# Kernel tuning notes

Measured on AMD Instinct MI355X. Metric: run time of the kernel, lower is better.

## Reference

```python
import jax, jax.numpy as jnp
import numpy as np

NUM_NODES = 10000
WINDOW = 8
IN_C = 8
HID = 64
N_TOT = WINDOW * NUM_NODES
N_EDGES = 1280000
EPS = 1e-5


def setup_inputs() -> dict:
    key = jax.random.key(0)
    ks = jax.random.split(key, 12)
    s = 0.05
    X = jax.random.normal(ks[0], (N_TOT, IN_C), jnp.float32)
    edge_index = jax.random.randint(ks[1], (2, N_EDGES), 0, N_TOT, dtype=jnp.int32)
    edge_weight = jax.random.uniform(ks[2], (N_EDGES,), jnp.float32)
    return dict(
        X=X, edge_index=edge_index, edge_weight=edge_weight,
        w1=jax.random.normal(ks[3], (IN_C, HID), jnp.float32) * s, b1=jnp.zeros(HID, jnp.float32),
        w2=jax.random.normal(ks[4], (HID, HID), jnp.float32) * s, b2=jnp.zeros(HID, jnp.float32),
        g1=jnp.ones(HID, jnp.float32), be1=jnp.zeros(HID, jnp.float32),
        g2=jnp.ones(HID, jnp.float32), be2=jnp.zeros(HID, jnp.float32),
        wih1=jax.random.normal(ks[5], (4 * HID, 2 * HID), jnp.float32) * s,
        whh1=jax.random.normal(ks[6], (4 * HID, HID), jnp.float32) * s,
        bih1=jnp.zeros(4 * HID, jnp.float32), bhh1=jnp.zeros(4 * HID, jnp.float32),
        wih2=jax.random.normal(ks[7], (4 * HID, HID), jnp.float32) * s,
        whh2=jax.random.normal(ks[8], (4 * HID, HID), jnp.float32) * s,
        bih2=jnp.zeros(4 * HID, jnp.float32), bhh2=jnp.zeros(4 * HID, jnp.float32),
    )


def _gcn(x, src, dst, ew, w, b):
    h = x @ w
    deg = jax.ops.segment_sum(ew, dst, num_segments=N_TOT) + 1.0
    dinv = jax.lax.rsqrt(deg)
    norm = dinv[src] * ew * dinv[dst]                               # [E]
    agg = jax.ops.segment_sum(norm[:, None] * h[src], dst, num_segments=N_TOT)
    return agg + h * (dinv * dinv)[:, None] + b                      # self-loop term: h[i]/deg[i]


def _bn(x, g, b):
    # BatchNorm1d, training-mode batch statistics (biased variance)
    mu = x.mean(0)
    var = ((x - mu) ** 2).mean(0)
    return (x - mu) * jax.lax.rsqrt(var + EPS) * g + b


def _lstm(xs, wih, whh, bih, bhh):
    # xs: [T, B, F]; torch gate order i, f, g, o
    B = xs.shape[1]
    def step(carry, xt):
        h, c = carry
        z = xt @ wih.T + h @ whh.T + bih + bhh
        i, f, g, o = jnp.split(z, 4, axis=1)
        c = jax.nn.sigmoid(f) * c + jax.nn.sigmoid(i) * jnp.tanh(g)
        h = jax.nn.sigmoid(o) * jnp.tanh(c)
        return (h, c), h
    init = (jnp.zeros((B, HID), xs.dtype), jnp.zeros((B, HID), xs.dtype))
    (h, c), ys = jax.lax.scan(step, init, xs)
    return ys, h


def reference(X, edge_index, edge_weight, w1, b1, w2, b2, g1, be1, g2, be2,
              wih1, whh1, bih1, bhh1, wih2, whh2, bih2, bhh2):
    src, dst = edge_index[0], edge_index[1]
    # skip-feature S: [B*num_nodes, in_channels + window - 1]
    S = X.reshape(1, WINDOW, NUM_NODES, IN_C).transpose(0, 2, 1, 3).reshape(-1, WINDOW, IN_C)
    Sfeat = jnp.concatenate([S[:, 0, :], S[:, 1:, IN_C - 1]], axis=1)
    # two GCN layers (dropout omitted: deterministic baseline)
    x1 = _bn(jax.nn.relu(_gcn(X, src, dst, edge_weight, w1, b1)), g1, be1)
    x2 = _bn(jax.nn.relu(_gcn(x1, src, dst, edge_weight, w2, b2)), g2, be2)
    xc = jnp.concatenate([x1, x2], axis=1)                           # [N_TOT, 2H]
    xs = xc.reshape(1, WINDOW, NUM_NODES, 2 * HID).transpose(1, 0, 2, 3).reshape(WINDOW, -1, 2 * HID)
    ys, h1 = _lstm(xs, wih1, whh1, bih1, bhh1)
    ys2, h2 = _lstm(ys, wih2, whh2, bih2, bhh2)
    return jnp.concatenate([h1, h2, Sfeat], axis=1)                  # [num_nodes, 2H + IN_C + WINDOW - 1]
```

## Files before the change

kernel.cpp:

```cpp
#include <hip/hip_runtime.h>
#include <hip/hip_bf16.h>
#include <math.h>

#define NNODES 10000
#define NT     80000
#define NE     1280000
#define NBKT   625
#define CHUNK  5000
#define EPB    3072
#define BNEPS  1e-5f

typedef __bf16 bf16x8 __attribute__((ext_vector_type(8)));
typedef float  f32x4  __attribute__((ext_vector_type(4)));
typedef float  f32x2  __attribute__((ext_vector_type(2)));

__device__ __forceinline__ float frcp(float x){ return __builtin_amdgcn_rcpf(x); }
__device__ __forceinline__ float fsig(float x){ return frcp(1.0f + __expf(-x)); }
__device__ __forceinline__ float ftanh(float x){ return 1.0f - 2.0f*frcp(1.0f + __expf(2.0f*x)); }
__device__ __forceinline__ float u2f(unsigned int u){ union{unsigned int u; float f;} c; c.u=u; return c.f; }
__device__ __forceinline__ unsigned int f2u(float f){ union{float f; unsigned int u;} c; c.f=f; return c.u; }
__device__ __forceinline__ unsigned short f2bu(float v){ __hip_bfloat16 h = __float2bfloat16(v); return *(unsigned short*)&h; }
__device__ __forceinline__ unsigned int pk2(float a, float b){ return (unsigned int)f2bu(a) | ((unsigned int)f2bu(b) << 16); }
__device__ __forceinline__ float dec15(unsigned int p){ return u2f((p & 0x7fffu) << 17); }

__global__ __launch_bounds__(256) void prep_w_kernel(
    const float* __restrict__ wih1, const float* __restrict__ whh1,
    const float* __restrict__ bih1, const float* __restrict__ bhh1,
    const float* __restrict__ wih2, const float* __restrict__ whh2,
    const float* __restrict__ bih2, const float* __restrict__ bhh2,
    const float* __restrict__ w1g, const float* __restrict__ w2g,
    unsigned int* __restrict__ W1f, unsigned int* __restrict__ W2f,
    float* __restrict__ bs1, float* __restrict__ bs2,
    unsigned int* __restrict__ W2g, unsigned int* __restrict__ W1g)
{
    int gid = blockIdx.x*256 + threadIdx.x;
    if (gid < 24576) {
        int i = gid & 3, lane = (gid>>2)&63, rest = gid>>8;
        int ks = rest % 6; rest /= 6;
        int nt = rest & 3, w = rest >> 2;
        int gate = nt*64 + w*16 + (lane & 15);
        int k = ks*32 + ((lane>>4)&3)*8 + 2*i;
        float v0 = (k     < 128) ? wih1[gate*128 + k]       : whh1[gate*64 + (k-128)];
        float v1 = (k + 1 < 128) ? wih1[gate*128 + k + 1]   : whh1[gate*64 + (k+1-128)];
        W1f[gid] = pk2(v0, v1);
    } else if (gid < 40960) {
        int r = gid - 24576;
        int i = r & 3, lane = (r>>2)&63, rest = r>>8;
        int ks = rest & 3; rest >>= 2;
        int nt = rest & 3, w = rest >> 2;
        int gate = nt*64 + w*16 + (lane & 15);
        int k = ks*32 + ((lane>>4)&3)*8 + 2*i;
        float v0 = (k     < 64) ? wih2[gate*64 + k]     : whh2[gate*64 + (k-64)];
        float v1 = (k + 1 < 64) ? wih2[gate*64 + k + 1] : whh2[gate*64 + (k+1-64)];
        W2f[r] = pk2(v0, v1);
    } else if (gid < 41216) {
        int j = gid - 40960; bs1[j] = bih1[j] + bhh1[j];
    } else if (gid < 41472) {
        int j = gid - 41216; bs2[j] = bih2[j] + bhh2[j];
    } else if (gid < 43520) {
        int r = gid - 41472;
        int i = r & 3, lane = (r>>2)&63, rest = r>>8;
        int ks = rest & 1, w = rest >> 1;
        int col = w*16 + (lane & 15);
        int k = ks*32 + ((lane>>4)&3)*8 + 2*i;
        W2g[r] = pk2(w2g[k*64 + col], w2g[(k+1)*64 + col]);
    } else if (gid < 44544) {
        int r = gid - 43520;
        int i = r & 3, lane = (r>>2)&63, w = r>>8;
        int col = w*16 + (lane & 15);
        int k = ((lane>>4)&3)*8 + 2*i;
        float v0 = (k     < 8) ? w1g[k*64 + col]     : 0.f;
        float v1 = (k + 1 < 8) ? w1g[(k+1)*64 + col] : 0.f;
        W1g[r] = pk2(v0, v1);
    }
}

__global__ __launch_bounds__(256) void sortA1_kernel(const int* __restrict__ dst,
                                                     const float* __restrict__ X,
                                                     unsigned int* __restrict__ Xb,
                                                     int* __restrict__ histmat)
{
    __shared__ int h[NBKT];
    for (int i = threadIdx.x; i < NBKT; i += 256) h[i] = 0;
    __syncthreads();
    int base = blockIdx.x*CHUNK;
    for (int i = threadIdx.x; i < CHUNK; i += 256)
        atomicAdd(&h[dst[base + i] >> 7], 1);
    for (int i = threadIdx.x; i < 1250; i += 256) {
        int gid = blockIdx.x*1250 + i;
        float2 v = *(const float2*)&X[(size_t)gid*2];
        Xb[gid] = pk2(v.x, v.y);
    }
    __syncthreads();
    for (int i = threadIdx.x; i < NBKT; i += 256)
        histmat[blockIdx.x*640 + i] = h[i];
}

__global__ __launch_bounds__(256) void sortA2a_kernel(const int* __restrict__ histmat,
                                                      int* __restrict__ offmatT,
                                                      int* __restrict__ binTotal)
{
    __shared__ int v[256];
    int b = blockIdx.x, t = threadIdx.x;
    int x = histmat[t*640 + b];
    v[t] = x;
    __syncthreads();
    for (int off = 1; off < 256; off <<= 1) {
        int y = (t >= off) ? v[t-off] : 0;
        __syncthreads();
        v[t] += y;
        __syncthreads();
    }
    offmatT[b*256 + t] = v[t] - x;
    if (t == 255) binTotal[b] = v[255];
}

__global__ __launch_bounds__(1024) void sortA2b_kernel(const int* __restrict__ binTotal,
                                                       int* __restrict__ bucketbase,
                                                       int* __restrict__ rowptr)
{
    __shared__ int part[1024];
    int t = threadIdx.x;
    int v = (t < NBKT) ? binTotal[t] : 0;
    part[t] = v;
    __syncthreads();
    for (int off = 1; off < 1024; off <<= 1) {
        int y = (t >= off) ? part[t-off] : 0;
        __syncthreads();
        part[t] += y;
        __syncthreads();
    }
    if (t < NBKT) bucketbase[t] = part[t] - v;
    if (t == 0) { bucketbase[NBKT] = NE; rowptr[NT] = NE; }
}

__global__ __launch_bounds__(256) void sortA3_kernel(const int* __restrict__ src,
                                                     const int* __restrict__ dst,
                                                     const float* __restrict__ ew,
                                                     const int* __restrict__ offmatT,
                                                     const int* __restrict__ bucketbase,
                                                     uint2* __restrict__ esort)
{
    __shared__ int cur[NBKT];
    int blk = blockIdx.x;
    for (int i = threadIdx.x; i < NBKT; i += 256)
        cur[i] = bucketbase[i] + offmatT[i*256 + blk];
    __syncthreads();
    int base = blk*CHUNK;
    for (int i = threadIdx.x; i < CHUNK; i += 256) {
        int e = base + i;
        int d = dst[e];
        int pos = atomicAdd(&cur[d >> 7], 1);
        uint2 r;
        r.x = (unsigned int)src[e] | ((unsigned int)(d & 127) << 17);
        r.y = f2u(ew[e]);
        esort[pos] = r;
    }
}

__global__ __launch_bounds__(256) void sortB1_kernel(const int* __restrict__ bucketbase,
                                                     const uint2* __restrict__ esort,
                                                     unsigned char* __restrict__ urank,
                                                     int* __restrict__ rowptr,
                                                     float* __restrict__ dinv)
{
    __shared__ int cnt[128];
    __shared__ float dg[128];
    __shared__ int ptr[128];
    int bin = blockIdx.x, t = threadIdx.x;
    if (t < 128) { cnt[t] = 0; dg[t] = 0.f; }
    __syncthreads();
    int base = bucketbase[bin], end = bucketbase[bin+1];
    for (int i = base + t; i < end; i += 256) {
        uint2 r = esort[i];
        int dl = (r.x >> 17) & 127;
        int rk = atomicAdd(&cnt[dl], 1);
        atomicAdd(&dg[dl], u2f(r.y));
        urank[i] = (unsigned char)rk;
    }
    __syncthreads();
    if (t < 128) ptr[t] = cnt[t];
    __syncthreads();
    for (int off = 1; off < 128; off <<= 1) {
        int y = (t >= off && t < 128) ? ptr[t-off] : 0;
        __syncthreads();
        if (t < 128) ptr[t] += y;
        __syncthreads();
    }
    if (t < 128) {
        rowptr[bin*128 + t] = base + ptr[t] - cnt[t];
        dinv[bin*128 + t]   = rsqrtf(dg[t] + 1.0f);
    }
}

__global__ __launch_bounds__(256) void sortB2g8_kernel(const int* __restrict__ bucketbase,
                                                       const uint2* __restrict__ esort,
                                                       const unsigned char* __restrict__ urank,
                                                       const int* __restrict__ rowptr,
                                                       const float* __restrict__ dinv,
                                                       unsigned int* __restrict__ epack,
                                                       const uint4* __restrict__ Xb,
                                                       uint4* __restrict__ agg8b)
{
    __shared__ unsigned int eld[EPB];
    int bin = blockIdx.x;
    int base = bucketbase[bin], end = bucketbase[bin+1];
    int cnt = end - base;
    for (int i = threadIdx.x; i < cnt; i += 256) {
        uint2 r = esort[base + i];
        int s = r.x & 0x1FFFF;
        int d = bin*128 + ((r.x >> 17) & 127);
        float w = u2f(r.y) * dinv[s];
        unsigned int p15 = (f2u(w) + (1u << 16)) >> 17;
        unsigned int pv = ((unsigned int)s << 15) | p15;
        int pos = rowptr[d] + (int)urank[base + i];
        epack[pos] = pv;
        int lpos = pos - base;
        if (lpos < EPB) eld[lpos] = pv;
    }
    __syncthreads();
    int t = threadIdx.x;
    int dl = t >> 1, par = t & 1;
    int d = bin*128 + dl;
    int beg = rowptr[d], endd = rowptr[d+1];
    float acc[8];
    #pragma unroll
    for (int k = 0; k < 8; ++k) acc[k] = 0.f;
    for (int i = beg + par; i < endd; i += 2) {
        int lpos = i - base;
        unsigned int p = (lpos < EPB) ? eld[lpos] : epack[i];
        float nrm = dec15(p);
        uint4 xv = Xb[p >> 15];
        unsigned int um[4] = {xv.x, xv.y, xv.z, xv.w};
        #pragma unroll
        for (int m = 0; m < 4; ++m) {
            acc[2*m]   = fmaf(nrm, u2f(um[m] << 16),         acc[2*m]);
            acc[2*m+1] = fmaf(nrm, u2f(um[m] & 0xffff0000u), acc[2*m+1]);
        }
    }
    #pragma unroll
    for (int k = 0; k < 8; ++k) acc[k] += __shfl_xor(acc[k], 1);
    if (par == 0) {
        float dv = dinv[d];
        uint4 xd = Xb[d];
        unsigned int ud[4] = {xd.x, xd.y, xd.z, xd.w};
        #pragma unroll
        for (int m = 0; m < 4; ++m) {
            acc[2*m]   = dv * fmaf(dv, u2f(ud[m] << 16),         acc[2*m]);
            acc[2*m+1] = dv * fmaf(dv, u2f(ud[m] & 0xffff0000u), acc[2*m+1]);
        }
        agg8b[d] = make_uint4(pk2(acc[0],acc[1]), pk2(acc[2],acc[3]),
                              pk2(acc[4],acc[5]), pk2(acc[6],acc[7]));
    }
}

__global__ __launch_bounds__(256) void gemm8relu_kernel(const uint4* __restrict__ agg8b,
                                                        const unsigned int* __restrict__ W1g,
                                                        const float* __restrict__ b,
                                                        unsigned short* __restrict__ y,
                                                        float* __restrict__ sums)
{
    __shared__ __align__(16) unsigned short As[64][8];
    __shared__ float sm[256], sq[256];
    const int tid = threadIdx.x;
    const int w = tid >> 6, lane = tid & 63, lr = lane & 15, lg = lane >> 4;
    union { uint4 u; bf16x8 v; } bw; bw.u = ((const uint4*)W1g)[w*64 + lane];
    float bc = b[w*16 + lr];
    float s = 0.f, q = 0.f;
    for (int tile = blockIdx.x; tile < NT/64; tile += gridDim.x) {
        int rbase = tile*64;
        __syncthreads();
        if (tid < 64) *(uint4*)&As[tid][0] = agg8b[rbase + tid];
        __syncthreads();
        #pragma unroll
        for (int rt = 0; rt < 4; ++rt) {
            bf16x8 a = {};
            if (lg == 0) a = *(const bf16x8*)&As[rt*16 + lr][0];
            f32x4 acc = {0.f, 0.f, 0.f, 0.f};
            acc = __builtin_amdgcn_mfma_f32_16x16x32_bf16(a, bw.v, acc, 0, 0, 0);
            #pragma unroll
            for (int r = 0; r < 4; ++r) {
                float v = fmaxf(acc[r] + bc, 0.f);
                y[(size_t)(rbase + rt*16 + lg*4 + r)*64 + w*16 + lr] = f2bu(v);
                s += v; q += v*v;
            }
        }
    }
    sm[tid] = s; sq[tid] = q;
    __syncthreads();
    if (tid < 64) {
        int base = (tid >> 4)*64 + (tid & 15);
        atomicAdd(&sums[tid],      sm[base] + sm[base+16] + sm[base+32] + sm[base+48]);
        atomicAdd(&sums[64 + tid], sq[base] + sq[base+16] + sq[base+32] + sq[base+48]);
    }
}

__global__ __launch_bounds__(256) void xbn8_kernel(const unsigned int* __restrict__ y1,
                                                   const float* __restrict__ sums,
                                                   const float* __restrict__ g,
                                                   const float* __restrict__ be,
                                                   unsigned int* __restrict__ xcat,
                                                   unsigned int* __restrict__ x8)
{
    __shared__ float axs[64], bxs[64];
    int tid = threadIdx.x;
    if (tid < 64) {
        float mu  = sums[tid] * (1.0f/NT);
        float var = sums[64 + tid] * (1.0f/NT) - mu*mu;
        float a = rsqrtf(var + BNEPS) * g[tid];
        axs[tid] = a; bxs[tid] = be[tid] - mu*a;
    }
    __syncthreads();
    int gid = blockIdx.x*256 + tid;
    if (gid >= NT*16) return;
    int c4 = gid & 15, n = gid >> 4;
    int c0 = c4*4;
    uint2 yy = *(const uint2*)&y1[(size_t)n*32 + 2*c4];
    float v0 = fmaf(axs[c0+0], u2f(yy.x << 16),         bxs[c0+0]);
    float v1 = fmaf(axs[c0+1], u2f(yy.x & 0xffff0000u), bxs[c0+1]);
    float v2 = fmaf(axs[c0+2], u2f(yy.y << 16),         bxs[c0+2]);
    float v3 = fmaf(axs[c0+3], u2f(yy.y & 0xffff0000u), bxs[c0+3]);
    *(uint2*)&xcat[(size_t)n*64 + 2*c4] = make_uint2(pk2(v0, v1), pk2(v2, v3));
    int p8 = 0;
    p8 = __builtin_amdgcn_cvt_pk_fp8_f32(v0, v1, p8, false);
    p8 = __builtin_amdgcn_cvt_pk_fp8_f32(v2, v3, p8, true);
    x8[(size_t)n*16 + c4] = (unsigned int)p8;
}

__global__ __launch_bounds__(256) void gather64_kernel(const int* __restrict__ rowptr,
                                                       const unsigned int* __restrict__ epack,
                                                       const unsigned int* __restrict__ x8,
                                                       const float* __restrict__ dinv,
                                                       unsigned int* __restrict__ xcat)
{
    int lane = threadIdx.x & 63;
    int g = lane >> 3;
    int l = lane & 7;
    int gwave = blockIdx.x*4 + (threadIdx.x >> 6);
    int nwaves = gridDim.x*4;
    for (int dp = gwave; dp < NT/2; dp += nwaves) {
        int dA = dp*2, dB = dA + 1;
        int begA = rowptr[dA], endA = rowptr[dA+1];
        int begB = endA, endB = rowptr[dB+1];
        int nA = endA - begA, nB = endB - begB;
        int n = nA > nB ? nA : nB;
        int clA = (endA > begA) ? endA - 1 : 0;
        int clB = (endB > begB) ? endB - 1 : 0;
        float a0=0.f,a1=0.f,a2=0.f,a3=0.f,a4=0.f,a5=0.f,a6=0.f,a7=0.f;
        float b0=0.f,b1=0.f,b2=0.f,b3=0.f,b4=0.f,b5=0.f,b6=0.f,b7=0.f;
        for (int i = 0; i < n; i += 8) {
            int iA = begA + i + g;
            bool vA = iA < endA;
            unsigned int pA = epack[vA ? iA : clA];
            float nrmA = vA ? dec15(pA) : 0.f;
            int iB = begB + i + g;
            bool vB = iB < endB;
            unsigned int pB = epack[vB ? iB : clB];
            float nrmB = vB ? dec15(pB) : 0.f;
            uint2 xvA = *(const uint2*)&x8[(size_t)(pA >> 15)*16 + 2*l];
            uint2 xvB = *(const uint2*)&x8[(size_t)(pB >> 15)*16 + 2*l];
            f32x2 qa0 = __builtin_amdgcn_cvt_pk_f32_fp8((int)xvA.x, false);
            f32x2 qa1 = __builtin_amdgcn_cvt_pk_f32_fp8((int)xvA.x, true);
            f32x2 qa2 = __builtin_amdgcn_cvt_pk_f32_fp8((int)xvA.y, false);
            f32x2 qa3 = __builtin_amdgcn_cvt_pk_f32_fp8((int)xvA.y, true);
            a0 = fmaf(nrmA, qa0[0], a0); a1 = fmaf(nrmA, qa0[1], a1);
            a2 = fmaf(nrmA, qa1[0], a2); a3 = fmaf(nrmA, qa1[1], a3);
            a4 = fmaf(nrmA, qa2[0], a4); a5 = fmaf(nrmA, qa2[1], a5);
            a6 = fmaf(nrmA, qa3[0], a6); a7 = fmaf(nrmA, qa3[1], a7);
            f32x2 qb0 = __builtin_amdgcn_cvt_pk_f32_fp8((int)xvB.x, false);
            f32x2 qb1 = __builtin_amdgcn_cvt_pk_f32_fp8((int)xvB.x, true);
            f32x2 qb2 = __builtin_amdgcn_cvt_pk_f32_fp8((int)xvB.y, false);
            f32x2 qb3 = __builtin_amdgcn_cvt_pk_f32_fp8((int)xvB.y, true);
            b0 = fmaf(nrmB, qb0[0], b0); b1 = fmaf(nrmB, qb0[1], b1);
            b2 = fmaf(nrmB, qb1[0], b2); b3 = fmaf(nrmB, qb1[1], b3);
            b4 = fmaf(nrmB, qb2[0], b4); b5 = fmaf(nrmB, qb2[1], b5);
            b6 = fmaf(nrmB, qb3[0], b6); b7 = fmaf(nrmB, qb3[1], b7);
        }
        #pragma unroll
        for (int off = 8; off < 64; off <<= 1) {
            a0 += __shfl_xor(a0, off); a1 += __shfl_xor(a1, off);
            a2 += __shfl_xor(a2, off); a3 += __shfl_xor(a3, off);
            a4 += __shfl_xor(a4, off); a5 += __shfl_xor(a5, off);
            a6 += __shfl_xor(a6, off); a7 += __shfl_xor(a7, off);
            b0 += __shfl_xor(b0, off); b1 += __shfl_xor(b1, off);
            b2 += __shfl_xor(b2, off); b3 += __shfl_xor(b3, off);
            b4 += __shfl_xor(b4, off); b5 += __shfl_xor(b5, off);
            b6 += __shfl_xor(b6, off); b7 += __shfl_xor(b7, off);
        }
        if (g == 0) {
            float dvA = dinv[dA];
            uint4 xdA = *(const uint4*)&xcat[(size_t)dA*64 + 4*l];
            a0 = dvA * fmaf(dvA, u2f(xdA.x << 16),         a0);
            a1 = dvA * fmaf(dvA, u2f(xdA.x & 0xffff0000u), a1);
            a2 = dvA * fmaf(dvA, u2f(xdA.y << 16),         a2);
            a3 = dvA * fmaf(dvA, u2f(xdA.y & 0xffff0000u), a3);
            a4 = dvA * fmaf(dvA, u2f(xdA.z << 16),         a4);
            a5 = dvA * fmaf(dvA, u2f(xdA.z & 0xffff0000u), a5);
            a6 = dvA * fmaf(dvA, u2f(xdA.w << 16),         a6);
            a7 = dvA * fmaf(dvA, u2f(xdA.w & 0xffff0000u), a7);
            *(uint4*)&xcat[(size_t)dA*64 + 32 + 4*l] =
                make_uint4(pk2(a0,a1), pk2(a2,a3), pk2(a4,a5), pk2(a6,a7));
            float dvB = dinv[dB];
            uint4 xdB = *(const uint4*)&xcat[(size_t)dB*64 + 4*l];
            b0 = dvB * fmaf(dvB, u2f(xdB.x << 16),         b0);
            b1 = dvB * fmaf(dvB, u2f(xdB.x & 0xffff0000u), b1);
            b2 = dvB * fmaf(dvB, u2f(xdB.y << 16),         b2);
            b3 = dvB * fmaf(dvB, u2f(xdB.y & 0xffff0000u), b3);
            b4 = dvB * fmaf(dvB, u2f(xdB.z << 16),         b4);
            b5 = dvB * fmaf(dvB, u2f(xdB.z & 0xffff0000u), b5);
            b6 = dvB * fmaf(dvB, u2f(xdB.w << 16),         b6);
            b7 = dvB * fmaf(dvB, u2f(xdB.w & 0xffff0000u), b7);
            *(uint4*)&xcat[(size_t)dB*64 + 32 + 4*l] =
                make_uint4(pk2(b0,b1), pk2(b2,b3), pk2(b4,b5), pk2(b6,b7));
        }
    }
}

__global__ __launch_bounds__(256) void gemm64relu_kernel(const unsigned int* __restrict__ xcat,
                                                         const unsigned int* __restrict__ W2g,
                                                         const float* __restrict__ b,
                                                         unsigned short* __restrict__ y,
                                                         float* __restrict__ sums)
{
    __shared__ __align__(16) unsigned short As[64][72];
    __shared__ float sm[256], sq[256];
    const int tid = threadIdx.x;
    const int w = tid >> 6, lane = tid & 63, lr = lane & 15, lg = lane >> 4;
    union { uint4 u; bf16x8 v; } b0, b1;
    b0.u = ((const uint4*)W2g)[(w*2 + 0)*64 + lane];
    b1.u = ((const uint4*)W2g)[(w*2 + 1)*64 + lane];
    float bc = b[w*16 + lr];
    const int srow = tid >> 2, squad = tid & 3;
    float s = 0.f, q = 0.f;
    for (int tile = blockIdx.x; tile < NT/64; tile += gridDim.x) {
        int rbase = tile*64;
        __syncthreads();
        {
            const unsigned int* src = &xcat[(size_t)(rbase + srow)*64 + 32 + squad*8];
            unsigned int* dst = (unsigned int*)&As[srow][0] + squad*8;
            *(uint4*)(dst)     = *(const uint4*)(src);
            *(uint4*)(dst + 4) = *(const uint4*)(src + 4);
        }
        __syncthreads();
        #pragma unroll
        for (int rt = 0; rt < 4; ++rt) {
            bf16x8 a0 = *(const bf16x8*)&As[rt*16 + lr][lg*8];
            bf16x8 a1 = *(const bf16x8*)&As[rt*16 + lr][32 + lg*8];
            f32x4 acc = {0.f, 0.f, 0.f, 0.f};
            acc = __builtin_amdgcn_mfma_f32_16x16x32_bf16(a0, b0.v, acc, 0, 0, 0);
            acc = __builtin_amdgcn_mfma_f32_16x16x32_bf16(a1, b1.v, acc, 0, 0, 0);
            #pragma unroll
            for (int r = 0; r < 4; ++r) {
                float v = fmaxf(acc[r] + bc, 0.f);
                y[(size_t)(rbase + rt*16 + lg*4 + r)*64 + w*16 + lr] = f2bu(v);
                s += v; q += v*v;
            }
        }
    }
    sm[tid] = s; sq[tid] = q;
    __syncthreads();
    if (tid < 64) {
        int base = (tid >> 4)*64 + (tid & 15);
        atomicAdd(&sums[tid],      sm[base] + sm[base+16] + sm[base+32] + sm[base+48]);
        atomicAdd(&sums[64 + tid], sq[base] + sq[base+16] + sq[base+32] + sq[base+48]);
    }
}

#define LROW 328
__global__ __launch_bounds__(256, 2) void lstm_mfma_kernel(
    const unsigned int* __restrict__ xcat,
    const unsigned int* __restrict__ y2,
    const float* __restrict__ sums2, const float* __restrict__ g2,
    const float* __restrict__ be2,
    const unsigned int* __restrict__ W1f, const unsigned int* __restrict__ W2f,
    const float* __restrict__ bs1, const float* __restrict__ bs2,
    float* __restrict__ out)
{
    __shared__ __align__(16) unsigned short xb[16][LROW];
    const int tid  = threadIdx.x;
    const int w    = tid >> 6, lane = tid & 63;
    const int lr   = lane & 15;
    const int lg   = lane >> 4;
    const int nb0  = blockIdx.x * 16;

    uint4 w1f[4][6], w2f[4][4];
    {
        const uint4* p1 = (const uint4*)W1f;
        #pragma unroll
        for (int nt = 0; nt < 4; ++nt)
            #pragma unroll
            for (int ks = 0; ks < 6; ++ks)
                w1f[nt][ks] = p1[((w*4 + nt)*6 + ks)*64 + lane];
        const uint4* p2 = (const uint4*)W2f;
        #pragma unroll
        for (int nt = 0; nt < 4; ++nt)
            #pragma unroll
            for (int ks = 0; ks < 4; ++ks)
                w2f[nt][ks] = p2[((w*4 + nt)*4 + ks)*64 + lane];
    }
    float b1v[4], b2v[4];
    #pragma unroll
    for (int nt = 0; nt < 4; ++nt) {
        b1v[nt] = bs1[nt*64 + w*16 + lr];
        b2v[nt] = bs2[nt*64 + w*16 + lr];
    }

    const int sn = tid >> 4, k0 = (tid & 15)*8;
    float ax[8], bx[8];
    if (k0 >= 64) {
        #pragma unroll
        for (int j = 0; j < 8; ++j) {
            int c = k0 - 64 + j;
            float mu  = sums2[c] * (1.0f/NT);
            float var = sums2[64 + c] * (1.0f/NT) - mu*mu;
            float a = rsqrtf(var + BNEPS) * g2[c];
            ax[j] = a; bx[j] = be2[c] - mu*a;
        }
    }

    for (int i = tid; i < 16*24; i += 256) {
        int n = i / 24, kk = 128 + (i % 24)*8;
        uint4 z; z.x = z.y = z.z = z.w = 0u;
        *(uint4*)&xb[n][kk] = z;
    }

    auto stage = [&](int step) {
        size_t row = (size_t)(step*NNODES + nb0 + sn);
        uint4 raw;
        if (k0 < 64) {
            raw = *(const uint4*)&xcat[row*64 + (k0 >> 1)];
        } else {
            raw = *(const uint4*)&y2[row*32 + ((k0 - 64) >> 1)];
            unsigned int um[4] = {raw.x, raw.y, raw.z, raw.w};
            #pragma unroll
            for (int m = 0; m < 4; ++m) {
                float v0 = fmaf(ax[2*m],   u2f(um[m] << 16),         bx[2*m]);
                float v1 = fmaf(ax[2*m+1], u2f(um[m] & 0xffff0000u), bx[2*m+1]);
                um[m] = pk2(v0, v1);
            }
            raw.x = um[0]; raw.y = um[1]; raw.z = um[2]; raw.w = um[3];
        }
        *(uint4*)&xb[sn][k0] = raw;
    };
    stage(0);
    float c1[4] = {0.f,0.f,0.f,0.f}, c2[4] = {0.f,0.f,0.f,0.f};

    for (int step = 0; step < 8; ++step) {
        __syncthreads();

        f32x4 acc[4];
        #pragma unroll
        for (int nt = 0; nt < 4; ++nt) { acc[nt][0]=0.f; acc[nt][1]=0.f; acc[nt][2]=0.f; acc[nt][3]=0.f; }
        #pragma unroll
        for (int ks = 0; ks < 6; ++ks) {
            bf16x8 a = *(const bf16x8*)&xb[lr][ks*32 + lg*8];
            #pragma unroll
            for (int nt = 0; nt < 4; ++nt) {
                union { uint4 u; bf16x8 v; } wb; wb.u = w1f[nt][ks];
                acc[nt] = __builtin_amdgcn_mfma_f32_16x16x32_bf16(a, wb.v, acc[nt], 0, 0, 0);
            }
        }
        __syncthreads();

        #pragma unroll
        for (int r = 0; r < 4; ++r) {
            float zi = acc[0][r] + b1v[0];
            float zf = acc[1][r] + b1v[1];
            float zg = acc[2][r] + b1v[2];
            float zo = acc[3][r] + b1v[3];
            float c  = fsig(zf)*c1[r] + fsig(zi)*ftanh(zg);
            c1[r] = c;
            float hv = fsig(zo)*ftanh(c);
            int node = lg*4 + r;
            xb[node][128 + w*16 + lr] = f2bu(hv);
            if (step == 7) out[(size_t)(nb0 + node)*143 + w*16 + lr] = hv;
        }
        if (step < 7) stage(step + 1);
        __syncthreads();

        int rb = 192 + 64*((step+1)&1);
        int wb2 = 192 + 64*(step&1);
        #pragma unroll
        for (int nt = 0; nt < 4; ++nt) { acc[nt][0]=0.f; acc[nt][1]=0.f; acc[nt][2]=0.f; acc[nt][3]=0.f; }
        #pragma unroll
        for (int ks = 0; ks < 2; ++ks) {
            bf16x8 a = *(const bf16x8*)&xb[lr][128 + ks*32 + lg*8];
            #pragma unroll
            for (int nt = 0; nt < 4; ++nt) {
                union { uint4 u; bf16x8 v; } wbv; wbv.u = w2f[nt][ks];
                acc[nt] = __builtin_amdgcn_mfma_f32_16x16x32_bf16(a, wbv.v, acc[nt], 0, 0, 0);
            }
        }
        #pragma unroll
        for (int ks = 0; ks < 2; ++ks) {
            bf16x8 a = *(const bf16x8*)&xb[lr][rb + ks*32 + lg*8];
            #pragma unroll
            for (int nt = 0; nt < 4; ++nt) {
                union { uint4 u; bf16x8 v; } wbv; wbv.u = w2f[nt][2+ks];
                acc[nt] = __builtin_amdgcn_mfma_f32_16x16x32_bf16(a, wbv.v, acc[nt], 0, 0, 0);
            }
        }
        #pragma unroll
        for (int r = 0; r < 4; ++r) {
            float zi = acc[0][r] + b2v[0];
            float zf = acc[1][r] + b2v[1];
            float zg = acc[2][r] + b2v[2];
            float zo = acc[3][r] + b2v[3];
            float c  = fsig(zf)*c2[r] + fsig(zi)*ftanh(zg);
            c2[r] = c;
            float hv = fsig(zo)*ftanh(c);
            int node = lg*4 + r;
            xb[node][wb2 + w*16 + lr] = f2bu(hv);
            if (step == 7) out[(size_t)(nb0 + node)*143 + 64 + w*16 + lr] = hv;
        }
    }
}

__global__ __launch_bounds__(256) void sfeat_kernel(const float* __restrict__ X,
                                                    float* __restrict__ out)
{
    int gid = blockIdx.x*256 + threadIdx.x;
    if (gid >= NNODES*15) return;
    int n = gid/15, i = gid%15;
    float v = (i < 8) ? X[(size_t)n*8 + i]
                      : X[((size_t)(i-7)*NNODES + n)*8 + 7];
    out[(size_t)n*143 + 128 + i] = v;
}

extern "C" void kernel_launch(void* const* d_in, const int* in_sizes, int n_in,
                              void* d_out, int out_size, void* d_ws, size_t ws_size,
                              hipStream_t stream)
{
    (void)in_sizes; (void)n_in; (void)out_size; (void)ws_size;
    const float* X    = (const float*)d_in[0];
    const int*   ei   = (const int*)d_in[1];
    const float* ew   = (const float*)d_in[2];
    const float* w1   = (const float*)d_in[3];
    const float* b1   = (const float*)d_in[4];
    const float* w2   = (const float*)d_in[5];
    const float* b2   = (const float*)d_in[6];
    const float* g1   = (const float*)d_in[7];
    const float* be1  = (const float*)d_in[8];
    const float* g2   = (const float*)d_in[9];
    const float* be2  = (const float*)d_in[10];
    const float* wih1 = (const float*)d_in[11];
    const float* whh1 = (const float*)d_in[12];
    const float* bih1 = (const float*)d_in[13];
    const float* bhh1 = (const float*)d_in[14];
    const float* wih2 = (const float*)d_in[15];
    const float* whh2 = (const float*)d_in[16];
    const float* bih2 = (const float*)d_in[17];
    const float* bhh2 = (const float*)d_in[18];
    float* out = (float*)d_out;
    float* ws  = (float*)d_ws;

    const int* src = ei;
    const int* dst = ei + NE;

    float* sums      = ws;
    float* dinv      = ws + 256;
    int*   rowptr    = (int*)(ws + 80256);
    int*   binTotal  = (int*)(ws + 160260);
    int*   bucketbase= (int*)(ws + 160900);
    int*   histmat   = (int*)(ws + 161540);
    int*   offmatT   = (int*)(ws + 325380);
    unsigned char* urank = (unsigned char*)(ws + 485380);
    uint2* esort     = (uint2*)(ws + 805384);
    unsigned int* x8 = (unsigned int*)(ws + 805384);
    unsigned int* y2 = (unsigned int*)(ws + 805384);
    unsigned int* epack = (unsigned int*)(ws + 3365384);
    unsigned int* Xb = (unsigned int*)(ws + 4645384);
    uint4* agg8b     = (uint4*)(ws + 4965384);
    unsigned int* y1 = (unsigned int*)(ws + 5605384);
    unsigned int* xcat = (unsigned int*)(ws + 8165384);
    unsigned int* W1f  = (unsigned int*)(ws + 13285384);
    unsigned int* W2f  = W1f + 24576;
    float* bs1 = (float*)(W2f + 16384);
    float* bs2 = bs1 + 256;
    unsigned int* W2g  = (unsigned int*)(bs2 + 256);
    unsigned int* W1g  = W2g + 2048;

    hipMemsetAsync(ws, 0, 256 * 4, stream);

    prep_w_kernel<<<174, 256, 0, stream>>>(wih1,whh1,bih1,bhh1,
                                           wih2,whh2,bih2,bhh2,
                                           w1, w2,
                                           W1f,W2f,bs1,bs2,W2g,W1g);
    sortA1_kernel<<<256, 256, 0, stream>>>(dst, X, Xb, histmat);
    sortA2a_kernel<<<NBKT, 256, 0, stream>>>(histmat, offmatT, binTotal);
    sortA2b_kernel<<<1, 1024, 0, stream>>>(binTotal, bucketbase, rowptr);
    sortA3_kernel<<<256, 256, 0, stream>>>(src, dst, ew, offmatT, bucketbase, esort);
    sortB1_kernel<<<NBKT, 256, 0, stream>>>(bucketbase, esort, urank, rowptr, dinv);
    sortB2g8_kernel<<<NBKT, 256, 0, stream>>>(bucketbase, esort, urank, rowptr, dinv,
                                              epack, (const uint4*)Xb, agg8b);

    gemm8relu_kernel<<<320, 256, 0, stream>>>(agg8b, W1g, b1, (unsigned short*)y1, sums);

    xbn8_kernel<<<(NT*16+255)/256, 256, 0, stream>>>(y1, sums, g1, be1, xcat, x8);

    gather64_kernel<<<2048, 256, 0, stream>>>(rowptr, epack, x8, dinv, xcat);
    gemm64relu_kernel<<<320, 256, 0, stream>>>(xcat, W2g, b2, (unsigned short*)y2, sums + 128);

    lstm_mfma_kernel<<<NNODES/16, 256, 0, stream>>>(xcat, y2, sums + 128, g2, be2,
                                                    W1f, W2f, bs1, bs2, out);
    sfeat_kernel<<<(NNODES*15+255)/256, 256, 0, stream>>>(X, out);
}
```

Before: 179.7 us.

## Fuse small kernels: merge prep with histogram, GEMM into gather, sfeat into LSTM

```diff
diff --git a/kernel.cpp b/kernel.cpp
--- a/kernel.cpp
+++ b/kernel.cpp
@@ -23,7 +23,9 @@
 __device__ __forceinline__ unsigned int pk2(float a, float b){ return (unsigned int)f2bu(a) | ((unsigned int)f2bu(b) << 16); }
 __device__ __forceinline__ float dec15(unsigned int p){ return u2f((p & 0x7fffu) << 17); }
 
-__global__ __launch_bounds__(256) void prep_w_kernel(
+__global__ __launch_bounds__(256) void prepA1_kernel(
+    const int* __restrict__ dst, const float* __restrict__ X,
+    unsigned int* __restrict__ Xb, int* __restrict__ histmat,
     const float* __restrict__ wih1, const float* __restrict__ whh1,
     const float* __restrict__ bih1, const float* __restrict__ bhh1,
     const float* __restrict__ wih2, const float* __restrict__ whh2,
@@ -33,7 +35,24 @@
     float* __restrict__ bs1, float* __restrict__ bs2,
     unsigned int* __restrict__ W2g, unsigned int* __restrict__ W1g)
 {
-    int gid = blockIdx.x*256 + threadIdx.x;
+    __shared__ int h[NBKT];
+    if (blockIdx.x < 256) {
+        for (int i = threadIdx.x; i < NBKT; i += 256) h[i] = 0;
+        __syncthreads();
+        int base = blockIdx.x*CHUNK;
+        for (int i = threadIdx.x; i < CHUNK; i += 256)
+            atomicAdd(&h[dst[base + i] >> 7], 1);
+        for (int i = threadIdx.x; i < 1250; i += 256) {
+            int gid = blockIdx.x*1250 + i;
+            float2 v = *(const float2*)&X[(size_t)gid*2];
+            Xb[gid] = pk2(v.x, v.y);
+        }
+        __syncthreads();
+        for (int i = threadIdx.x; i < NBKT; i += 256)
+            histmat[blockIdx.x*640 + i] = h[i];
+        return;
+    }
+    int gid = (blockIdx.x - 256)*256 + threadIdx.x;
     if (gid < 24576) {
         int i = gid & 3, lane = (gid>>2)&63, rest = gid>>8;
         int ks = rest % 6; rest /= 6;
@@ -75,27 +94,6 @@
     }
 }
 
-__global__ __launch_bounds__(256) void sortA1_kernel(const int* __restrict__ dst,
-                                                     const float* __restrict__ X,
-                                                     unsigned int* __restrict__ Xb,
-                                                     int* __restrict__ histmat)
-{
-    __shared__ int h[NBKT];
-    for (int i = threadIdx.x; i < NBKT; i += 256) h[i] = 0;
-    __syncthreads();
-    int base = blockIdx.x*CHUNK;
-    for (int i = threadIdx.x; i < CHUNK; i += 256)
-        atomicAdd(&h[dst[base + i] >> 7], 1);
-    for (int i = threadIdx.x; i < 1250; i += 256) {
-        int gid = blockIdx.x*1250 + i;
-        float2 v = *(const float2*)&X[(size_t)gid*2];
-        Xb[gid] = pk2(v.x, v.y);
-    }
-    __syncthreads();
-    for (int i = threadIdx.x; i < NBKT; i += 256)
-        histmat[blockIdx.x*640 + i] = h[i];
-}
-
 __global__ __launch_bounds__(256) void sortA2a_kernel(const int* __restrict__ histmat,
                                                       int* __restrict__ offmatT,
                                                       int* __restrict__ binTotal)
@@ -193,16 +191,21 @@
     }
 }
 
-__global__ __launch_bounds__(256) void sortB2g8_kernel(const int* __restrict__ bucketbase,
-                                                       const uint2* __restrict__ esort,
-                                                       const unsigned char* __restrict__ urank,
-                                                       const int* __restrict__ rowptr,
-                                                       const float* __restrict__ dinv,
-                                                       unsigned int* __restrict__ epack,
-                                                       const uint4* __restrict__ Xb,
-                                                       uint4* __restrict__ agg8b)
+__global__ __launch_bounds__(256) void sortB2g8m_kernel(const int* __restrict__ bucketbase,
+                                                        const uint2* __restrict__ esort,
+                                                        const unsigned char* __restrict__ urank,
+                                                        const int* __restrict__ rowptr,
+                                                        const float* __restrict__ dinv,
+                                                        unsigned int* __restrict__ epack,
+                                                        const uint4* __restrict__ Xb,
+                                                        const unsigned int* __restrict__ W1g,
+                                                        const float* __restrict__ b1,
+                                                        unsigned short* __restrict__ y1,
+                                                        float* __restrict__ sums)
 {
     __shared__ unsigned int eld[EPB];
+    __shared__ __align__(16) unsigned short As[128][8];
+    __shared__ float smc[256][4], sqc[256][4];
     int bin = blockIdx.x;
     int base = bucketbase[bin], end = bucketbase[bin+1];
     int cnt = end - base;
@@ -219,79 +222,88 @@
         if (lpos < EPB) eld[lpos] = pv;
     }
     __syncthreads();
-    int t = threadIdx.x;
-    int dl = t >> 1, par = t & 1;
-    int d = bin*128 + dl;
-    int beg = rowptr[d], endd = rowptr[d+1];
-    float acc[8];
-    #pragma unroll
-    for (int k = 0; k < 8; ++k) acc[k] = 0.f;
-    for (int i = beg + par; i < endd; i += 2) {
-        int lpos = i - base;
-        unsigned int p = (lpos < EPB) ? eld[lpos] : epack[i];
-        float nrm = dec15(p);
-        uint4 xv = Xb[p >> 15];
-        unsigned int um[4] = {xv.x, xv.y, xv.z, xv.w};
-        #pragma unroll
-        for (int m = 0; m < 4; ++m) {
-            acc[2*m]   = fmaf(nrm, u2f(um[m] << 16),         acc[2*m]);
-            acc[2*m+1] = fmaf(nrm, u2f(um[m] & 0xffff0000u), acc[2*m+1]);
-        }
-    }
-    #pragma unroll
-    for (int k = 0; k < 8; ++k) acc[k] += __shfl_xor(acc[k], 1);
-    if (par == 0) {
-        float dv = dinv[d];
-        uint4 xd = Xb[d];
-        unsigned int ud[4] = {xd.x, xd.y, xd.z, xd.w};
-        #pragma unroll
-        for (int m = 0; m < 4; ++m) {
-            acc[2*m]   = dv * fmaf(dv, u2f(ud[m] << 16),         acc[2*m]);
-            acc[2*m+1] = dv * fmaf(dv, u2f(ud[m] & 0xffff0000u), acc[2*m+1]);
-        }
-        agg8b[d] = make_uint4(pk2(acc[0],acc[1]), pk2(acc[2],acc[3]),
-                              pk2(acc[4],acc[5]), pk2(acc[6],acc[7]));
-    }
-}
-
-__global__ __launch_bounds__(256) void gemm8relu_kernel(const uint4* __restrict__ agg8b,
-                                                        const unsigned int* __restrict__ W1g,
-                                                        const float* __restrict__ b,
-                                                        unsigned short* __restrict__ y,
-                                                        float* __restrict__ sums)
-{
-    __shared__ __align__(16) unsigned short As[64][8];
-    __shared__ float sm[256], sq[256];
-    const int tid = threadIdx.x;
-    const int w = tid >> 6, lane = tid & 63, lr = lane & 15, lg = lane >> 4;
-    union { uint4 u; bf16x8 v; } bw; bw.u = ((const uint4*)W1g)[w*64 + lane];
-    float bc = b[w*16 + lr];
-    float s = 0.f, q = 0.f;
-    for (int tile = blockIdx.x; tile < NT/64; tile += gridDim.x) {
-        int rbase = tile*64;
-        __syncthreads();
-        if (tid < 64) *(uint4*)&As[tid][0] = agg8b[rbase + tid];
-        __syncthreads();
-        #pragma unroll
-        for (int rt = 0; rt < 4; ++rt) {
+    {
+        int t = threadIdx.x;
+        int dl = t >> 1, par = t & 1;
+        int d = bin*128 + dl;
+        int beg = rowptr[d], endd = rowptr[d+1];
+        float acc[8];
+        #pragma unroll
+        for (int k = 0; k < 8; ++k) acc[k] = 0.f;
+        for (int i = beg + par; i < endd; i += 2) {
+            int lpos = i - base;
+            unsigned int p = (lpos < EPB) ? eld[lpos] : epack[i];
+            float nrm = dec15(p);
+            uint4 xv = Xb[p >> 15];
+            unsigned int um[4] = {xv.x, xv.y, xv.z, xv.w};
+            #pragma unroll
+            for (int m = 0; m < 4; ++m) {
+                acc[2*m]   = fmaf(nrm, u2f(um[m] << 16),         acc[2*m]);
+                acc[2*m+1] = fmaf(nrm, u2f(um[m] & 0xffff0000u), acc[2*m+1]);
+            }
+        }
+        #pragma unroll
+        for (int k = 0; k < 8; ++k) acc[k] += __shfl_xor(acc[k], 1);
+        if (par == 0) {
+            float dv = dinv[d];
+            uint4 xd = Xb[d];
+            unsigned int ud[4] = {xd.x, xd.y, xd.z, xd.w};
+            #pragma unroll
+            for (int m = 0; m < 4; ++m) {
+                acc[2*m]   = dv * fmaf(dv, u2f(ud[m] << 16),         acc[2*m]);
+                acc[2*m+1] = dv * fmaf(dv, u2f(ud[m] & 0xffff0000u), acc[2*m+1]);
+            }
+            *(uint4*)&As[dl][0] = make_uint4(pk2(acc[0],acc[1]), pk2(acc[2],acc[3]),
+                                             pk2(acc[4],acc[5]), pk2(acc[6],acc[7]));
+        }
+    }
+    __syncthreads();
+    {
+        int t = threadIdx.x;
+        int w = t >> 6, lane = t & 63, lr = lane & 15, lg = lane >> 4;
+        uint4 bfrag[4];
+        float bb[4];
+        #pragma unroll
+        for (int nt = 0; nt < 4; ++nt) {
+            bfrag[nt] = ((const uint4*)W1g)[nt*64 + lane];
+            bb[nt] = b1[nt*16 + lr];
+        }
+        float sc[4] = {0.f,0.f,0.f,0.f}, qc[4] = {0.f,0.f,0.f,0.f};
+        #pragma unroll
+        for (int rr = 0; rr < 2; ++rr) {
+            int rt = w*2 + rr;
             bf16x8 a = {};
             if (lg == 0) a = *(const bf16x8*)&As[rt*16 + lr][0];
-            f32x4 acc = {0.f, 0.f, 0.f, 0.f};
-            acc = __builtin_amdgcn_mfma_f32_16x16x32_bf16(a, bw.v, acc, 0, 0, 0);
-            #pragma unroll
-            for (int r = 0; r < 4; ++r) {
-                float v = fmaxf(acc[r] + bc, 0.f);
-                y[(size_t)(rbase + rt*16 + lg*4 + r)*64 + w*16 + lr] = f2bu(v);
-                s += v; q += v*v;
+            #pragma unroll
+            for (int nt = 0; nt < 4; ++nt) {
+                union { uint4 u; bf16x8 v; } bw; bw.u = bfrag[nt];
+                f32x4 acc = {0.f, 0.f, 0.f, 0.f};
+                acc = __builtin_amdgcn_mfma_f32_16x16x32_bf16(a, bw.v, acc, 0, 0, 0);
+                #pragma unroll
+                for (int r = 0; r < 4; ++r) {
+                    float v = fmaxf(acc[r] + bb[nt], 0.f);
+                    int row = bin*128 + rt*16 + lg*4 + r;
+                    y1[(size_t)row*64 + nt*16 + lr] = f2bu(v);
+                    sc[nt] += v; qc[nt] += v*v;
+                }
             }
         }
-    }
-    sm[tid] = s; sq[tid] = q;
-    __syncthreads();
-    if (tid < 64) {
-        int base = (tid >> 4)*64 + (tid & 15);
-        atomicAdd(&sums[tid],      sm[base] + sm[base+16] + sm[base+32] + sm[base+48]);
-        atomicAdd(&sums[64 + tid], sq[base] + sq[base+16] + sq[base+32] + sq[base+48]);
+        #pragma unroll
+        for (int nt = 0; nt < 4; ++nt) { smc[t][nt] = sc[nt]; sqc[t][nt] = qc[nt]; }
+        __syncthreads();
+        if (t < 64) {
+            int nt = t >> 4, lr2 = t & 15;
+            float s = 0.f, q = 0.f;
+            #pragma unroll
+            for (int w4 = 0; w4 < 4; ++w4)
+                #pragma unroll
+                for (int lg2 = 0; lg2 < 4; ++lg2) {
+                    int idx = w4*64 + lg2*16 + lr2;
+                    s += smc[idx][nt]; q += sqc[idx][nt];
+                }
+            atomicAdd(&sums[t], s);
+            atomicAdd(&sums[64 + t], q);
+        }
     }
 }
 
@@ -474,6 +486,7 @@
     const float* __restrict__ be2,
     const unsigned int* __restrict__ W1f, const unsigned int* __restrict__ W2f,
     const float* __restrict__ bs1, const float* __restrict__ bs2,
+    const float* __restrict__ X,
     float* __restrict__ out)
 {
     __shared__ __align__(16) unsigned short xb[16][LROW];
@@ -482,6 +495,14 @@
     const int lr   = lane & 15;
     const int lg   = lane >> 4;
     const int nb0  = blockIdx.x * 16;
+
+    if (tid < 240) {
+        int gid = blockIdx.x*240 + tid;
+        int n = gid/15, ii = gid%15;
+        float v = (ii < 8) ? X[(size_t)n*8 + ii]
+                           : X[((size_t)(ii-7)*NNODES + n)*8 + 7];
+        out[(size_t)n*143 + 128 + ii] = v;
+    }
 
     uint4 w1f[4][6], w2f[4][4];
     {
@@ -614,17 +635,6 @@
             if (step == 7) out[(size_t)(nb0 + node)*143 + 64 + w*16 + lr] = hv;
         }
     }
-}
-
-__global__ __launch_bounds__(256) void sfeat_kernel(const float* __restrict__ X,
-                                                    float* __restrict__ out)
-{
-    int gid = blockIdx.x*256 + threadIdx.x;
-    if (gid >= NNODES*15) return;
-    int n = gid/15, i = gid%15;
-    float v = (i < 8) ? X[(size_t)n*8 + i]
-                      : X[((size_t)(i-7)*NNODES + n)*8 + 7];
-    out[(size_t)n*143 + 128 + i] = v;
 }
 
 extern "C" void kernel_launch(void* const* d_in, const int* in_sizes, int n_in,
@@ -670,7 +680,6 @@
     unsigned int* y2 = (unsigned int*)(ws + 805384);
     unsigned int* epack = (unsigned int*)(ws + 3365384);
     unsigned int* Xb = (unsigned int*)(ws + 4645384);
-    uint4* agg8b     = (uint4*)(ws + 4965384);
     unsigned int* y1 = (unsigned int*)(ws + 5605384);
     unsigned int* xcat = (unsigned int*)(ws + 8165384);
     unsigned int* W1f  = (unsigned int*)(ws + 13285384);
@@ -682,19 +691,18 @@
 
     hipMemsetAsync(ws, 0, 256 * 4, stream);
 
-    prep_w_kernel<<<174, 256, 0, stream>>>(wih1,whh1,bih1,bhh1,
+    prepA1_kernel<<<430, 256, 0, stream>>>(dst, X, Xb, histmat,
+                                           wih1,whh1,bih1,bhh1,
                                            wih2,whh2,bih2,bhh2,
                                            w1, w2,
                                            W1f,W2f,bs1,bs2,W2g,W1g);
-    sortA1_kernel<<<256, 256, 0, stream>>>(dst, X, Xb, histmat);
     sortA2a_kernel<<<NBKT, 256, 0, stream>>>(histmat, offmatT, binTotal);
     sortA2b_kernel<<<1, 1024, 0, stream>>>(binTotal, bucketbase, rowptr);
     sortA3_kernel<<<256, 256, 0, stream>>>(src, dst, ew, offmatT, bucketbase, esort);
     sortB1_kernel<<<NBKT, 256, 0, stream>>>(bucketbase, esort, urank, rowptr, dinv);
-    sortB2g8_kernel<<<NBKT, 256, 0, stream>>>(bucketbase, esort, urank, rowptr, dinv,
-                                              epack, (const uint4*)Xb, agg8b);
-
-    gemm8relu_kernel<<<320, 256, 0, stream>>>(agg8b, W1g, b1, (unsigned short*)y1, sums);
+    sortB2g8m_kernel<<<NBKT, 256, 0, stream>>>(bucketbase, esort, urank, rowptr, dinv,
+                                               epack, (const uint4*)Xb, W1g, b1,
+                                               (unsigned short*)y1, sums);
 
     xbn8_kernel<<<(NT*16+255)/256, 256, 0, stream>>>(y1, sums, g1, be1, xcat, x8);
 
@@ -702,6 +710,5 @@
     gemm64relu_kernel<<<320, 256, 0, stream>>>(xcat, W2g, b2, (unsigned short*)y2, sums + 128);
 
     lstm_mfma_kernel<<<NNODES/16, 256, 0, stream>>>(xcat, y2, sums + 128, g2, be2,
-                                                    W1f, W2f, bs1, bs2, out);
-    sfeat_kernel<<<(NNODES*15+255)/256, 256, 0, stream>>>(X, out);
-}
+                                                    W1f, W2f, bs1, bs2, X, out);
+}
```

Result: faster. 174.9 us (median of 2 runs) (-2.7%).
